# Performance work log

Measured on AMD Instinct MI355X. Metric: run time of the kernel, lower is better.

The kernel has to match this reference:

```python
import math
import jax, jax.numpy as jnp
import numpy as np

WS = 16        # window size (square)
SHIFT = 8      # window_size // 2 (window_shift=True)
NUM_HEADS = 6

def _rel_coords_table(ws):
    # Swin-V2 log-spaced continuous relative coords, shape (1, 2ws-1, 2ws-1, 2)
    r = np.arange(-(ws - 1), ws, dtype=np.float32)
    t = np.stack(np.meshgrid(r, r, indexing='ij'), axis=-1)[None]
    t = t / (ws - 1) * 8.0
    t = np.sign(t) * np.log2(np.abs(t) + 1.0) / np.log2(8.0)
    return t.astype(np.float32)

def _rel_pos_index(ws):
    ch, cw = np.meshgrid(np.arange(ws), np.arange(ws), indexing='ij')
    coords = np.stack([ch.ravel(), cw.ravel()])          # (2, N)
    rel = coords[:, :, None] - coords[:, None, :]        # (2, N, N)
    rel = rel.transpose(1, 2, 0).astype(np.int64)
    rel[..., 0] += ws - 1
    rel[..., 1] += ws - 1
    rel[..., 0] *= 2 * ws - 1
    return rel.sum(-1).astype(np.int32)                  # (N, N), values in [0, (2ws-1)^2)

def _shift_mask(H, W, ws, shift):
    img = np.zeros((H, W), dtype=np.float32)
    cnt = 0
    for hs in (slice(0, -ws), slice(-ws, -shift), slice(-shift, None)):
        for wsl in (slice(0, -ws), slice(-ws, -shift), slice(-shift, None)):
            img[hs, wsl] = cnt; cnt += 1
    win = img.reshape(H // ws, ws, W // ws, ws).transpose(0, 2, 1, 3).reshape(-1, ws * ws)
    diff = win[:, None, :] - win[:, :, None]
    return np.where(diff != 0, -100.0, 0.0).astype(np.float32)  # (nW, N, N)

def setup_inputs():
    key = jax.random.key(0)
    ks = jax.random.split(key, 4)
    B, H, W = 16, 64, 64
    C = 3 * NUM_HEADS * 32  # 576 (qkv channels)
    qkv = jax.random.normal(ks[0], (B, H * W, C), dtype=jnp.float32)
    table = jnp.asarray(_rel_coords_table(WS))
    index = jnp.asarray(_rel_pos_index(WS))
    mask = jnp.asarray(_shift_mask(H, W, WS, SHIFT))
    logit_scale = jnp.log(10.0 * jnp.ones((NUM_HEADS, 1, 1), dtype=jnp.float32))
    w1 = jax.random.normal(ks[1], (512, 2), dtype=jnp.float32) * 0.02
    b1 = jnp.zeros((512,), dtype=jnp.float32)
    w2 = jax.random.normal(ks[2], (NUM_HEADS, 512), dtype=jnp.float32) * 0.02
    return {"qkv": qkv, "table": table, "mask": mask, "logit_scale": logit_scale,
            "w1": w1, "b1": b1, "w2": w2, "index": index, "H": H, "W": W}

def reference(qkv, table, mask, logit_scale, w1, b1, w2, index, H, W):
    B, L, C = qkv.shape
    dim = C // 3
    hd = dim // NUM_HEADS
    x = qkv.reshape(B, H, W, C)
    x = jnp.roll(x, (-SHIFT, -SHIFT), axis=(1, 2))
    nWh, nWw = H // WS, W // WS
    # window partition -> (B_, N, C)
    x = x.reshape(B, nWh, WS, nWw, WS, C).transpose(0, 1, 3, 2, 4, 5).reshape(-1, WS * WS, C)
    B_, N, _ = x.shape
    qkv_ = x.reshape(B_, N, 3, NUM_HEADS, hd).transpose(2, 0, 3, 1, 4)
    q, k, v = qkv_[0], qkv_[1], qkv_[2]  # (B_, H, N, hd)
    # cosine attention
    qn = q / jnp.maximum(jnp.linalg.norm(q, axis=-1, keepdims=True), 1e-12)
    kn = k / jnp.maximum(jnp.linalg.norm(k, axis=-1, keepdims=True), 1e-12)
    attn = jnp.einsum('bhnd,bhmd->bhnm', qn, kn)
    scale = jnp.exp(jnp.minimum(logit_scale, math.log(1.0 / 0.01)))  # (H,1,1)
    attn = attn * scale[None]
    # CPB MLP bias: Linear(2,512)+ReLU -> Linear(512,H,no bias)
    hidden = jax.nn.relu(table @ w1.T + b1)          # (1, 2ws-1, 2ws-1, 512)
    bias_table = (hidden @ w2.T).reshape(-1, NUM_HEADS)
    bias = bias_table[index.reshape(-1)].reshape(N, N, NUM_HEADS).transpose(2, 0, 1)
    attn = attn + 16.0 * jax.nn.sigmoid(bias)[None]
    # shifted-window mask
    nWm = mask.shape[0]
    attn = attn.reshape(B_ // nWm, nWm, NUM_HEADS, N, N) + mask[None, :, None]
    attn = attn.reshape(B_, NUM_HEADS, N, N)
    attn = jax.nn.softmax(attn, axis=-1)
    out = jnp.einsum('bhnm,bhmd->bhnd', attn, v)
    out = out.transpose(0, 2, 1, 3).reshape(B_, N, dim)
    # window reverse + unshift
    out = out.reshape(B, nWh, nWw, WS, WS, dim).transpose(0, 1, 3, 2, 4, 5).reshape(B, H, W, dim)
    out = jnp.roll(out, (SHIFT, SHIFT), axis=(1, 2))
    return out.reshape(B, L, dim)
```

## Files before the change

### kernel.cpp

```cpp
#include <hip/hip_runtime.h>
#include <cstdint>

#define NH 6
#define HD 32
#define NTOK 256
#define CIN 576
#define DIMO 192
#define LOG2E 1.44269504f
#define SHIFT2 37.6f
#define MNEG (-144.269504f)

typedef short short8 __attribute__((ext_vector_type(8)));
typedef float f32x4 __attribute__((ext_vector_type(4)));

__device__ __forceinline__ int grp6(int x) { return (x < 48) ? 0 : ((x < 56) ? 1 : 2); }

__device__ __forceinline__ unsigned short f2bf(float f) {
    unsigned int u = __float_as_uint(f);
    u += 0x7fffu + ((u >> 16) & 1u);
    return (unsigned short)(u >> 16);
}
__device__ __forceinline__ float bf2f(unsigned short s) {
    return __uint_as_float(((unsigned)s) << 16);
}

__global__ void cpb_kernel(const float* __restrict__ table,
                           const float* __restrict__ w1,
                           const float* __restrict__ b1,
                           const float* __restrict__ w2,
                           float* __restrict__ bv) {
    __shared__ float hid[512];
    int p = blockIdx.x;
    float t0 = table[2 * p], t1 = table[2 * p + 1];
    int t = threadIdx.x;
    for (int j = t; j < 512; j += 256) {
        float hv = fmaf(t0, w1[2 * j], fmaf(t1, w1[2 * j + 1], b1[j]));
        hid[j] = fmaxf(hv, 0.f);
    }
    __syncthreads();
    if (t < 192) {
        int h = t >> 5, l = t & 31;
        const float* w2h = w2 + h * 512;
        float acc = 0.f;
        for (int j = l; j < 512; j += 32) acc = fmaf(hid[j], w2h[j], acc);
        acc += __shfl_xor(acc, 1, 32);
        acc += __shfl_xor(acc, 2, 32);
        acc += __shfl_xor(acc, 4, 32);
        acc += __shfl_xor(acc, 8, 32);
        acc += __shfl_xor(acc, 16, 32);
        if (l == 0) bv[h * 961 + p] = (16.f / (1.f + __expf(-acc))) * LOG2E;
    }
}

__global__ __launch_bounds__(512, 4) void attn_kernel(
    const float* __restrict__ qkv,
    const float* __restrict__ logit_scale,
    const float* __restrict__ bv,
    float* __restrict__ out)
{
    __shared__ __align__(16) short Qb[NTOK * HD];
    __shared__ __align__(16) short Kb[NTOK * HD];
    __shared__ __align__(16) short Vt[HD * 264];
    __shared__ __align__(16) short P[8 * 32 * 32];
    __shared__ float Bv[961];

    const int t = threadIdx.x;
    const int h = blockIdx.x % NH;
    const int win = blockIdx.x / NH;
    const int b = win >> 4, wl = win & 15, wh = wl >> 2, ww = wl & 3;

    const float scale2 = __expf(fminf(logit_scale[h], 4.6051702f)) * LOG2E;

    for (int p = t; p < 961; p += 512) Bv[p] = bv[h * 961 + p];

    {
        int n = (t < 256) ? t : (t - 256);
        int i = n >> 4, j = n & 15;
        int rr = wh * 16 + i, cc = ww * 16 + j;
        int r = (rr + 8) & 63, c = (cc + 8) & 63;
        const float* base = qkv + ((long)(b * 4096 + r * 64 + c)) * CIN + h * HD;
        if (t < 256) {
            float qv[32], kv[32];
            const float4* qp = (const float4*)base;
            const float4* kp = (const float4*)(base + DIMO);
#pragma unroll
            for (int w = 0; w < 8; ++w) {
                float4 x = qp[w];
                qv[4 * w + 0] = x.x; qv[4 * w + 1] = x.y; qv[4 * w + 2] = x.z; qv[4 * w + 3] = x.w;
            }
#pragma unroll
            for (int w = 0; w < 8; ++w) {
                float4 x = kp[w];
                kv[4 * w + 0] = x.x; kv[4 * w + 1] = x.y; kv[4 * w + 2] = x.z; kv[4 * w + 3] = x.w;
            }
            float sq = 0.f, sk = 0.f;
#pragma unroll
            for (int d = 0; d < 32; ++d) { sq = fmaf(qv[d], qv[d], sq); sk = fmaf(kv[d], kv[d], sk); }
            float qs = scale2 / fmaxf(sqrtf(sq), 1e-12f);
            float ks = 1.f / fmaxf(sqrtf(sk), 1e-12f);
#pragma unroll
            for (int w = 0; w < 4; ++w) {
                short8 qc, kc;
#pragma unroll
                for (int e = 0; e < 8; ++e) {
                    qc[e] = (short)f2bf(qv[8 * w + e] * qs);
                    kc[e] = (short)f2bf(kv[8 * w + e] * ks);
                }
                *(short8*)&Qb[n * 32 + 8 * w] = qc;
                *(short8*)&Kb[n * 32 + 8 * w] = kc;
            }
        } else {
            float vv[32];
            const float4* vp = (const float4*)(base + 2 * DIMO);
#pragma unroll
            for (int w = 0; w < 8; ++w) {
                float4 x = vp[w];
                vv[4 * w + 0] = x.x; vv[4 * w + 1] = x.y; vv[4 * w + 2] = x.z; vv[4 * w + 3] = x.w;
            }
#pragma unroll
            for (int d = 0; d < 32; ++d) Vt[d * 264 + n] = (short)f2bf(vv[d]);
        }
    }
    __syncthreads();

    const int wv = t >> 6, lane = t & 63, quad = lane >> 4, l15 = lane & 15;
    short* Pw = P + wv * 1024;

    int trg[2];
    short8 aQ[2];
#pragma unroll
    for (int tl = 0; tl < 2; ++tl) {
        trg[tl] = wv * 2 + tl;
        aQ[tl] = *(const short8*)&Qb[(trg[tl] * 16 + l15) * 32 + quad * 8];
    }
    int gqi[2];
#pragma unroll
    for (int tl = 0; tl < 2; ++tl) gqi[tl] = grp6(wh * 16 + trg[tl]);
    int gqj[4];
#pragma unroll
    for (int reg = 0; reg < 4; ++reg) gqj[reg] = grp6(ww * 16 + quad * 4 + reg);
    const int gmj = grp6(ww * 16 + l15);

    f32x4 O[2][2];
    float lp[2][4];
#pragma unroll
    for (int tl = 0; tl < 2; ++tl)
#pragma unroll
        for (int dtk = 0; dtk < 2; ++dtk) O[tl][dtk] = (f32x4){0.f, 0.f, 0.f, 0.f};
#pragma unroll
    for (int tl = 0; tl < 2; ++tl)
#pragma unroll
        for (int reg = 0; reg < 4; ++reg) lp[tl][reg] = 0.f;

    const f32x4 Zero = (f32x4){0.f, 0.f, 0.f, 0.f};

    for (int c = 0; c < 8; ++c) {
        short8 bK[2];
        int gmi[2], ctg[2];
#pragma unroll
        for (int ct = 0; ct < 2; ++ct) {
            ctg[ct] = c * 2 + ct;
            bK[ct] = *(const short8*)&Kb[(ctg[ct] * 16 + l15) * 32 + quad * 8];
            gmi[ct] = grp6(wh * 16 + ctg[ct]);
        }
        f32x4 S[2][2];
#pragma unroll
        for (int tl = 0; tl < 2; ++tl)
#pragma unroll
            for (int ct = 0; ct < 2; ++ct)
                S[tl][ct] = __builtin_amdgcn_mfma_f32_16x16x32_bf16(aQ[tl], bK[ct], Zero, 0, 0, 0);

#pragma unroll
        for (int tl = 0; tl < 2; ++tl) {
#pragma unroll
            for (int ct = 0; ct < 2; ++ct) {
                int rbase = (trg[tl] - ctg[ct] + 15) * 31 + 15 - l15;
                bool mi = (gqi[tl] == gmi[ct]);
#pragma unroll
                for (int reg = 0; reg < 4; ++reg) {
                    float bias = Bv[rbase + quad * 4 + reg];
                    float mterm = (mi && (gqj[reg] == gmj)) ? 0.f : MNEG;
                    float arg = S[tl][ct][reg] + bias + mterm - SHIFT2;
                    float e = __builtin_amdgcn_exp2f(arg);
                    unsigned short pb = f2bf(e);
                    lp[tl][reg] += bf2f(pb);
                    Pw[(tl * 16 + quad * 4 + reg) * 32 + ct * 16 + l15] = (short)pb;
                }
            }
        }

        short8 aP[2], bV[2];
#pragma unroll
        for (int tl = 0; tl < 2; ++tl)
            aP[tl] = *(const short8*)&Pw[(tl * 16 + l15) * 32 + quad * 8];
#pragma unroll
        for (int dtk = 0; dtk < 2; ++dtk)
            bV[dtk] = *(const short8*)&Vt[(dtk * 16 + l15) * 264 + c * 32 + quad * 8];
#pragma unroll
        for (int tl = 0; tl < 2; ++tl)
#pragma unroll
            for (int dtk = 0; dtk < 2; ++dtk)
                O[tl][dtk] = __builtin_amdgcn_mfma_f32_16x16x32_bf16(aP[tl], bV[dtk], O[tl][dtk], 0, 0, 0);
    }

#pragma unroll
    for (int tl = 0; tl < 2; ++tl)
#pragma unroll
        for (int reg = 0; reg < 4; ++reg) {
            float s = lp[tl][reg];
            s += __shfl_xor(s, 1, 16);
            s += __shfl_xor(s, 2, 16);
            s += __shfl_xor(s, 4, 16);
            s += __shfl_xor(s, 8, 16);
            lp[tl][reg] = 1.f / s;
        }

    const long pixb = (long)b * 4096;
#pragma unroll
    for (int tl = 0; tl < 2; ++tl) {
        int r = (wh * 16 + trg[tl] + 8) & 63;
#pragma unroll
        for (int reg = 0; reg < 4; ++reg) {
            int cpix = (ww * 16 + quad * 4 + reg + 8) & 63;
            float* op = out + (pixb + r * 64 + cpix) * DIMO + h * HD + l15;
            float inv = lp[tl][reg];
            op[0]  = O[tl][0][reg] * inv;
            op[16] = O[tl][1][reg] * inv;
        }
    }
}

extern "C" void kernel_launch(void* const* d_in, const int* in_sizes, int n_in,
                              void* d_out, int out_size, void* d_ws, size_t ws_size,
                              hipStream_t stream) {
    const float* qkv         = (const float*)d_in[0];
    const float* table       = (const float*)d_in[1];
    const float* logit_scale = (const float*)d_in[3];
    const float* w1          = (const float*)d_in[4];
    const float* b1          = (const float*)d_in[5];
    const float* w2          = (const float*)d_in[6];
    float* out = (float*)d_out;
    float* bv  = (float*)d_ws;

    cpb_kernel<<<961, 256, 0, stream>>>(table, w1, b1, w2, bv);
    attn_kernel<<<256 * NH, 512, 0, stream>>>(qkv, logit_scale, bv, out);
}
```

Before: 264.8 us.

## Fold bias into MFMA accumulator and compute softmax row sums via MFMA

Expands the relative-position bias into a per-lane, MFMA-fragment-ordered LDS table with the exp shift pre-subtracted, and passes it as the accumulator input of the QK^T MFMA, which removes per-element bias loads and adds. Row sums are now produced by an extra MFMA against a ones vector instead of per-element accumulation plus cross-lane shuffles. bf16 rounding is simplified to round-half-up, and the P scratch buffer aliases the Q buffer once Q has been read into registers. In exchange, the bias table in LDS grows to about 31 KB, which may reduce occupancy, and the setup phase does more global loads.

Result: no change. 264.8 us (+0.0%).

```diff
diff --git a/kernel.cpp b/kernel.cpp
--- a/kernel.cpp
+++ b/kernel.cpp
@@ -19,9 +19,6 @@
     unsigned int u = __float_as_uint(f);
     u += 0x7fffu + ((u >> 16) & 1u);
     return (unsigned short)(u >> 16);
-}
-__device__ __forceinline__ float bf2f(unsigned short s) {
-    return __uint_as_float(((unsigned)s) << 16);
 }
 
 __global__ void cpb_kernel(const float* __restrict__ table,
@@ -58,11 +55,10 @@
     const float* __restrict__ bv,
     float* __restrict__ out)
 {
-    __shared__ __align__(16) short Qb[NTOK * HD];
     __shared__ __align__(16) short Kb[NTOK * HD];
     __shared__ __align__(16) short Vt[HD * 264];
-    __shared__ __align__(16) short P[8 * 32 * 32];
-    __shared__ float Bv[961];
+    __shared__ __align__(16) short QP[NTOK * HD];
+    __shared__ __align__(16) float Bf[31 * 256];
 
     const int t = threadIdx.x;
     const int h = blockIdx.x % NH;
@@ -71,7 +67,14 @@
 
     const float scale2 = __expf(fminf(logit_scale[h], 4.6051702f)) * LOG2E;
 
-    for (int p = t; p < 961; p += 512) Bv[p] = bv[h * 961 + p];
+    {
+        const float* bvh = bv + h * 961;
+        for (int idx = t; idx < 31 * 256; idx += 512) {
+            int d15 = idx >> 8, ln = (idx >> 2) & 63, rg = idx & 3;
+            int col = ((ln >> 4) * 4 + rg) - (ln & 15) + 15;
+            Bf[idx] = bvh[d15 * 31 + col] - SHIFT2;
+        }
+    }
 
     {
         int n = (t < 256) ? t : (t - 256);
@@ -106,7 +109,7 @@
                     qc[e] = (short)f2bf(qv[8 * w + e] * qs);
                     kc[e] = (short)f2bf(kv[8 * w + e] * ks);
                 }
-                *(short8*)&Qb[n * 32 + 8 * w] = qc;
+                *(short8*)&QP[n * 32 + 8 * w] = qc;
                 *(short8*)&Kb[n * 32 + 8 * w] = kc;
             }
         } else {
@@ -124,14 +127,14 @@
     __syncthreads();
 
     const int wv = t >> 6, lane = t & 63, quad = lane >> 4, l15 = lane & 15;
-    short* Pw = P + wv * 1024;
+    short* Pw = QP + wv * 1024;
 
     int trg[2];
     short8 aQ[2];
 #pragma unroll
     for (int tl = 0; tl < 2; ++tl) {
         trg[tl] = wv * 2 + tl;
-        aQ[tl] = *(const short8*)&Qb[(trg[tl] * 16 + l15) * 32 + quad * 8];
+        aQ[tl] = *(const short8*)&QP[(trg[tl] * 16 + l15) * 32 + quad * 8];
     }
     int gqi[2];
 #pragma unroll
@@ -141,18 +144,17 @@
     for (int reg = 0; reg < 4; ++reg) gqj[reg] = grp6(ww * 16 + quad * 4 + reg);
     const int gmj = grp6(ww * 16 + l15);
 
-    f32x4 O[2][2];
-    float lp[2][4];
-#pragma unroll
-    for (int tl = 0; tl < 2; ++tl)
+    f32x4 O[2][2], Osum[2];
+#pragma unroll
+    for (int tl = 0; tl < 2; ++tl) {
 #pragma unroll
         for (int dtk = 0; dtk < 2; ++dtk) O[tl][dtk] = (f32x4){0.f, 0.f, 0.f, 0.f};
-#pragma unroll
-    for (int tl = 0; tl < 2; ++tl)
-#pragma unroll
-        for (int reg = 0; reg < 4; ++reg) lp[tl][reg] = 0.f;
-
-    const f32x4 Zero = (f32x4){0.f, 0.f, 0.f, 0.f};
+        Osum[tl] = (f32x4){0.f, 0.f, 0.f, 0.f};
+    }
+
+    short8 bOne;
+#pragma unroll
+    for (int e = 0; e < 8; ++e) bOne[e] = (short)0x3F80;
 
     for (int c = 0; c < 8; ++c) {
         short8 bK[2];
@@ -167,28 +169,24 @@
 #pragma unroll
         for (int tl = 0; tl < 2; ++tl)
 #pragma unroll
-            for (int ct = 0; ct < 2; ++ct)
-                S[tl][ct] = __builtin_amdgcn_mfma_f32_16x16x32_bf16(aQ[tl], bK[ct], Zero, 0, 0, 0);
-
+            for (int ct = 0; ct < 2; ++ct) {
+                f32x4 Bfr = *(const f32x4*)&Bf[((trg[tl] - ctg[ct] + 15) << 8) + (lane << 2)];
+                S[tl][ct] = __builtin_amdgcn_mfma_f32_16x16x32_bf16(aQ[tl], bK[ct], Bfr, 0, 0, 0);
+            }
 #pragma unroll
         for (int tl = 0; tl < 2; ++tl) {
 #pragma unroll
             for (int ct = 0; ct < 2; ++ct) {
-                int rbase = (trg[tl] - ctg[ct] + 15) * 31 + 15 - l15;
                 bool mi = (gqi[tl] == gmi[ct]);
 #pragma unroll
                 for (int reg = 0; reg < 4; ++reg) {
-                    float bias = Bv[rbase + quad * 4 + reg];
                     float mterm = (mi && (gqj[reg] == gmj)) ? 0.f : MNEG;
-                    float arg = S[tl][ct][reg] + bias + mterm - SHIFT2;
-                    float e = __builtin_amdgcn_exp2f(arg);
-                    unsigned short pb = f2bf(e);
-                    lp[tl][reg] += bf2f(pb);
-                    Pw[(tl * 16 + quad * 4 + reg) * 32 + ct * 16 + l15] = (short)pb;
+                    float e = __builtin_amdgcn_exp2f(S[tl][ct][reg] + mterm);
+                    unsigned int u = __float_as_uint(e) + 0x8000u;
+                    Pw[(tl * 16 + quad * 4 + reg) * 32 + ct * 16 + l15] = (short)(u >> 16);
                 }
             }
         }
-
         short8 aP[2], bV[2];
 #pragma unroll
         for (int tl = 0; tl < 2; ++tl)
@@ -197,23 +195,13 @@
         for (int dtk = 0; dtk < 2; ++dtk)
             bV[dtk] = *(const short8*)&Vt[(dtk * 16 + l15) * 264 + c * 32 + quad * 8];
 #pragma unroll
-        for (int tl = 0; tl < 2; ++tl)
+        for (int tl = 0; tl < 2; ++tl) {
 #pragma unroll
             for (int dtk = 0; dtk < 2; ++dtk)
                 O[tl][dtk] = __builtin_amdgcn_mfma_f32_16x16x32_bf16(aP[tl], bV[dtk], O[tl][dtk], 0, 0, 0);
-    }
-
-#pragma unroll
-    for (int tl = 0; tl < 2; ++tl)
-#pragma unroll
-        for (int reg = 0; reg < 4; ++reg) {
-            float s = lp[tl][reg];
-            s += __shfl_xor(s, 1, 16);
-            s += __shfl_xor(s, 2, 16);
-            s += __shfl_xor(s, 4, 16);
-            s += __shfl_xor(s, 8, 16);
-            lp[tl][reg] = 1.f / s;
-        }
+            Osum[tl] = __builtin_amdgcn_mfma_f32_16x16x32_bf16(aP[tl], bOne, Osum[tl], 0, 0, 0);
+        }
+    }
 
     const long pixb = (long)b * 4096;
 #pragma unroll
@@ -223,7 +211,7 @@
         for (int reg = 0; reg < 4; ++reg) {
             int cpix = (ww * 16 + quad * 4 + reg + 8) & 63;
             float* op = out + (pixb + r * 64 + cpix) * DIMO + h * HD + l15;
-            float inv = lp[tl][reg];
+            float inv = 1.f / Osum[tl][reg];
             op[0]  = O[tl][0][reg] * inv;
             op[16] = O[tl][1][reg] * inv;
         }
```
